# Optimization experiments

Measured on AMD Instinct MI355X. Metric: run time of the kernel, lower is better.

Reference implementation:

```python
import jax, jax.numpy as jnp
import numpy as np

E = 64          # num_experts
D_IN = 512      # in_features
D_OUT = 512     # out_features
T = 262144      # total routed token-slots (grouped by expert, balanced)


def setup_inputs() -> dict:
    key = jax.random.key(0)
    k1, k2 = jax.random.split(key)
    STD = 0.02
    return {
        "input": jax.random.normal(k1, (T, D_IN), dtype=jnp.float32),
        # tokens are pre-grouped by expert; balanced routing -> equal counts
        "num_experts_per_token": jnp.full((E,), T // E, dtype=jnp.int64),
        "weight": jax.random.normal(k2, (E, D_OUT, D_IN), dtype=jnp.float32) * STD,
        "bias": jnp.zeros((E, D_OUT), dtype=jnp.float32),
    }


def reference(input, num_experts_per_token, weight, bias):
    # Faithful to the split + per-expert F.linear + cat path, for balanced
    # routing (equal counts per expert) so shapes are static under jit.
    e = weight.shape[0]
    tpe = input.shape[0] // e  # tokens per expert
    x = input.reshape(e, tpe, -1)                      # [E, tpe, D_in]
    # F.linear(x_e, W_e) = x_e @ W_e.T for each expert -> grouped GEMM
    out = jnp.einsum('eti,eoi->eto', x, weight)        # [E, tpe, D_out]
    out = out + bias[:, None, :]
    return out.reshape(e * tpe, -1)                    # [T, D_out]
```

## Files before the change

kernel.cpp:

```cpp
#include <hip/hip_runtime.h>
#include <hip/hip_bf16.h>


#define NEXPERT 64
#define DIN 512
#define DOUT 512
#define TPE 4096
#define BM 128
#define BN 256
#define BK 32
#define NKT (DIN / BK)

typedef __attribute__((ext_vector_type(8))) __bf16 bf16x8;
typedef __attribute__((ext_vector_type(4))) __bf16 bf16x4;
typedef __attribute__((ext_vector_type(4))) float f32x4;

__global__ __launch_bounds__(256, 2)
void moe_grouped_gemm(const float* __restrict__ x,
                      const float* __restrict__ w,
                      const float* __restrict__ bias,
                      float* __restrict__ out) {
  __shared__ __align__(16) unsigned char sA[2][BM * BK * 2];
  __shared__ __align__(16) unsigned char sB[2][BN * BK * 2];

  int bid = blockIdx.x;
  int swz = (bid & 7) * 512 + (bid >> 3);
  int e  = swz >> 6;
  int rr = swz & 63;
  int mt = rr >> 1;
  int nt = rr & 1;

  const int tid  = threadIdx.x;
  const int lane = tid & 63;
  const int wn   = tid >> 6;
  const int r15  = lane & 15;
  const int kg   = lane >> 4;

  const int c4 = tid & 7;
  const int tr = tid >> 3;
  const float* aG = x + ((size_t)e * TPE + (size_t)mt * BM + tr) * DIN + c4 * 4;
  const float* bG = w + ((size_t)e * DOUT + (size_t)nt * BN + tr) * DIN + c4 * 4;
  const int wrBase = tr * 64 + ((((c4 >> 1) ^ ((tr >> 1) & 3))) << 4) + (c4 & 1) * 8;

  const int chz = (kg ^ ((r15 >> 1) & 3)) << 4;
  const int aRd = r15 * 64 + chz;
  const int bRd = (wn * 64 + r15) * 64 + chz;

  f32x4 SA[4], SBv[8];

#define ISSUE(kt)                                                           \
  do {                                                                      \
    _Pragma("unroll") for (int i = 0; i < 4; ++i)                           \
      SA[i] = *(const f32x4*)(aG + (size_t)i * 32 * DIN + (kt) * BK);       \
    _Pragma("unroll") for (int i = 0; i < 8; ++i)                           \
      SBv[i] = *(const f32x4*)(bG + (size_t)i * 32 * DIN + (kt) * BK);      \
  } while (0)

#define WRITE(dbuf)                                                         \
  do {                                                                      \
    _Pragma("unroll") for (int i = 0; i < 4; ++i) {                         \
      bf16x4 c;                                                             \
      c[0] = (__bf16)SA[i][0]; c[1] = (__bf16)SA[i][1];                     \
      c[2] = (__bf16)SA[i][2]; c[3] = (__bf16)SA[i][3];                     \
      *(bf16x4*)(&sA[dbuf][wrBase + i * 2048]) = c;                         \
    }                                                                       \
    _Pragma("unroll") for (int i = 0; i < 8; ++i) {                         \
      bf16x4 c;                                                             \
      c[0] = (__bf16)SBv[i][0]; c[1] = (__bf16)SBv[i][1];                   \
      c[2] = (__bf16)SBv[i][2]; c[3] = (__bf16)SBv[i][3];                   \
      *(bf16x4*)(&sB[dbuf][wrBase + i * 2048]) = c;                         \
    }                                                                       \
  } while (0)

  f32x4 acc[8][4];
#pragma unroll
  for (int m = 0; m < 8; ++m)
#pragma unroll
    for (int n = 0; n < 4; ++n) acc[m][n] = (f32x4)0.f;

  ISSUE(0);
  WRITE(0);
  asm volatile("s_waitcnt lgkmcnt(0)" ::: "memory");
  __builtin_amdgcn_s_barrier();

#pragma unroll
  for (int t = 0; t < NKT; ++t) {
    const int d = t & 1;
    bf16x8 bfr[4], afl[4], afh[4];

#pragma unroll
    for (int ni = 0; ni < 4; ++ni)
      bfr[ni] = *(const bf16x8*)(&sB[d][bRd + ni * 1024]);
#pragma unroll
    for (int mi = 0; mi < 4; ++mi)
      afl[mi] = *(const bf16x8*)(&sA[d][aRd + mi * 1024]);
    if (t + 1 < NKT) ISSUE(t + 1);

    __builtin_amdgcn_s_barrier();
    __builtin_amdgcn_s_setprio(1);
#pragma unroll
    for (int mi = 0; mi < 4; ++mi)
#pragma unroll
      for (int ni = 0; ni < 4; ++ni)
        acc[mi][ni] = __builtin_amdgcn_mfma_f32_16x16x32_bf16(
            afl[mi], bfr[ni], acc[mi][ni], 0, 0, 0);
    __builtin_amdgcn_s_setprio(0);
    __builtin_amdgcn_s_barrier();

#pragma unroll
    for (int mi = 0; mi < 4; ++mi)
      afh[mi] = *(const bf16x8*)(&sA[d][aRd + 4096 + mi * 1024]);
    if (t + 1 < NKT) WRITE(d ^ 1);

    asm volatile("s_waitcnt lgkmcnt(0)" ::: "memory");
    __builtin_amdgcn_s_barrier();
    __builtin_amdgcn_s_setprio(1);
#pragma unroll
    for (int mi = 0; mi < 4; ++mi)
#pragma unroll
      for (int ni = 0; ni < 4; ++ni)
        acc[mi + 4][ni] = __builtin_amdgcn_mfma_f32_16x16x32_bf16(
            afh[mi], bfr[ni], acc[mi + 4][ni], 0, 0, 0);
    __builtin_amdgcn_s_setprio(0);
    __builtin_amdgcn_s_barrier();
  }

  float bv[4];
  const float* bp = bias + (size_t)e * DOUT + nt * BN + wn * 64 + r15;
#pragma unroll
  for (int n = 0; n < 4; ++n) bv[n] = bp[n * 16];

  const int q4 = (lane >> 4) * 4;
  float* Cb = out + ((size_t)e * TPE + (size_t)mt * BM) * DOUT + nt * BN + wn * 64;
#pragma unroll
  for (int m = 0; m < 8; ++m) {
#pragma unroll
    for (int j = 0; j < 4; ++j) {
      float* pr = Cb + (size_t)(m * 16 + q4 + j) * DOUT;
#pragma unroll
      for (int n = 0; n < 4; ++n)
        pr[n * 16 + r15] = acc[m][n][j] + bv[n];
    }
  }
#undef ISSUE
#undef WRITE
}

extern "C" void kernel_launch(void* const* d_in, const int* in_sizes, int n_in,
                              void* d_out, int out_size, void* d_ws, size_t ws_size,
                              hipStream_t stream) {
  const float* x    = (const float*)d_in[0];
  const float* w    = (const float*)d_in[2];
  const float* bias = (const float*)d_in[3];
  float* out        = (float*)d_out;

  dim3 grid(NEXPERT * (TPE / BM) * (DOUT / BN));
  dim3 block(256);
  hipLaunchKernelGGL(moe_grouped_gemm, grid, block, 0, stream, x, w, bias, out);
}
```

Measured before the change: 305.3 us.

## Pre-convert weights to bf16 and load B fragments directly into registers

Adds a pre-pass kernel that converts the fp32 expert weights to bf16 in workspace. The GEMM then loads B fragments straight from global memory into registers instead of staging them through LDS, and shares a single LDS barrier per k-step with A prefetched two steps ahead. This is meant to cut LDS traffic, barriers and conversion work in the main loop. The cost is an extra launch and roughly 32MB of extra weight traffic, plus global B reads that are not shared across the waves of a block.

```diff
diff --git a/kernel.cpp b/kernel.cpp
--- a/kernel.cpp
+++ b/kernel.cpp
@@ -15,18 +15,27 @@
 typedef __attribute__((ext_vector_type(4))) __bf16 bf16x4;
 typedef __attribute__((ext_vector_type(4))) float f32x4;
 
+__global__ __launch_bounds__(256)
+void convert_w_kernel(const float* __restrict__ w, __bf16* __restrict__ wb) {
+  size_t i = ((size_t)blockIdx.x * 256 + threadIdx.x) * 8;
+  f32x4 a = *(const f32x4*)(w + i);
+  f32x4 b = *(const f32x4*)(w + i + 4);
+  bf16x8 r;
+  r[0] = (__bf16)a[0]; r[1] = (__bf16)a[1]; r[2] = (__bf16)a[2]; r[3] = (__bf16)a[3];
+  r[4] = (__bf16)b[0]; r[5] = (__bf16)b[1]; r[6] = (__bf16)b[2]; r[7] = (__bf16)b[3];
+  *(bf16x8*)(wb + i) = r;
+}
+
+template <bool WB16>
 __global__ __launch_bounds__(256, 2)
-void moe_grouped_gemm(const float* __restrict__ x,
-                      const float* __restrict__ w,
-                      const float* __restrict__ bias,
-                      float* __restrict__ out) {
+void moe_gemm(const float* __restrict__ x, const void* __restrict__ wsrc,
+              const float* __restrict__ bias, float* __restrict__ out) {
   __shared__ __align__(16) unsigned char sA[2][BM * BK * 2];
-  __shared__ __align__(16) unsigned char sB[2][BN * BK * 2];
 
   int bid = blockIdx.x;
-  int swz = (bid & 7) * 512 + (bid >> 3);
-  int e  = swz >> 6;
-  int rr = swz & 63;
+  int swzb = (bid & 7) * 512 + (bid >> 3);
+  int e  = swzb >> 6;
+  int rr = swzb & 63;
   int mt = rr >> 1;
   int nt = rr & 1;
 
@@ -39,38 +48,47 @@
   const int c4 = tid & 7;
   const int tr = tid >> 3;
   const float* aG = x + ((size_t)e * TPE + (size_t)mt * BM + tr) * DIN + c4 * 4;
-  const float* bG = w + ((size_t)e * DOUT + (size_t)nt * BN + tr) * DIN + c4 * 4;
-  const int wrBase = tr * 64 + ((((c4 >> 1) ^ ((tr >> 1) & 3))) << 4) + (c4 & 1) * 8;
+  const int wrBase = tr * 64 + (((c4 >> 1) ^ ((tr >> 1) & 3)) << 4) + (c4 & 1) * 8;
 
   const int chz = (kg ^ ((r15 >> 1) & 3)) << 4;
   const int aRd = r15 * 64 + chz;
-  const int bRd = (wn * 64 + r15) * 64 + chz;
 
-  f32x4 SA[4], SBv[8];
+  const size_t bRow = (size_t)(e * DOUT + nt * BN + wn * 64 + r15) * DIN + kg * 8;
+  const __bf16* bPb = (const __bf16*)wsrc + bRow;
+  const float*  bPf = (const float*)wsrc + bRow;
 
-#define ISSUE(kt)                                                           \
-  do {                                                                      \
-    _Pragma("unroll") for (int i = 0; i < 4; ++i)                           \
-      SA[i] = *(const f32x4*)(aG + (size_t)i * 32 * DIN + (kt) * BK);       \
-    _Pragma("unroll") for (int i = 0; i < 8; ++i)                           \
-      SBv[i] = *(const f32x4*)(bG + (size_t)i * 32 * DIN + (kt) * BK);      \
-  } while (0)
+  f32x4 sa0[4], sa1[4];
+  bf16x8 b0v[4], b1v[4];
 
-#define WRITE(dbuf)                                                         \
-  do {                                                                      \
-    _Pragma("unroll") for (int i = 0; i < 4; ++i) {                         \
+#define ISSUEA(kt, Sr)                                                      \
+  { _Pragma("unroll") for (int i = 0; i < 4; ++i)                           \
+      Sr[i] = *(const f32x4*)(aG + (size_t)i * 32 * DIN + (kt) * BK); }
+
+#define WRITEA(dbuf, Sr)                                                    \
+  { _Pragma("unroll") for (int i = 0; i < 4; ++i) {                         \
       bf16x4 c;                                                             \
-      c[0] = (__bf16)SA[i][0]; c[1] = (__bf16)SA[i][1];                     \
-      c[2] = (__bf16)SA[i][2]; c[3] = (__bf16)SA[i][3];                     \
-      *(bf16x4*)(&sA[dbuf][wrBase + i * 2048]) = c;                         \
-    }                                                                       \
-    _Pragma("unroll") for (int i = 0; i < 8; ++i) {                         \
-      bf16x4 c;                                                             \
-      c[0] = (__bf16)SBv[i][0]; c[1] = (__bf16)SBv[i][1];                   \
-      c[2] = (__bf16)SBv[i][2]; c[3] = (__bf16)SBv[i][3];                   \
-      *(bf16x4*)(&sB[dbuf][wrBase + i * 2048]) = c;                         \
-    }                                                                       \
-  } while (0)
+      c[0] = (__bf16)Sr[i][0]; c[1] = (__bf16)Sr[i][1];                     \
+      c[2] = (__bf16)Sr[i][2]; c[3] = (__bf16)Sr[i][3];                     \
+      *(bf16x4*)(&sA[dbuf][wrBase + i * 2048]) = c; } }
+
+#define LOADB(kt, Br)                                                       \
+  { if constexpr (WB16) {                                                   \
+      _Pragma("unroll") for (int n = 0; n < 4; ++n)                         \
+        Br[n] = *(const bf16x8*)(bPb + (size_t)n * 16 * DIN + (kt) * BK);   \
+    } else {                                                                \
+      _Pragma("unroll") for (int n = 0; n < 4; ++n) {                       \
+        f32x4 lo = *(const f32x4*)(bPf + (size_t)n * 16 * DIN + (kt) * BK); \
+        f32x4 hi = *(const f32x4*)(bPf + (size_t)n * 16 * DIN + (kt) * BK + 4); \
+        bf16x8 rv;                                                          \
+        rv[0]=(__bf16)lo[0]; rv[1]=(__bf16)lo[1]; rv[2]=(__bf16)lo[2]; rv[3]=(__bf16)lo[3]; \
+        rv[4]=(__bf16)hi[0]; rv[5]=(__bf16)hi[1]; rv[6]=(__bf16)hi[2]; rv[7]=(__bf16)hi[3]; \
+        Br[n] = rv; } } }
+
+#define MFMAS(Bv)                                                           \
+  { _Pragma("unroll") for (int mi = 0; mi < 8; ++mi)                        \
+      _Pragma("unroll") for (int ni = 0; ni < 4; ++ni)                      \
+        acc[mi][ni] = __builtin_amdgcn_mfma_f32_16x16x32_bf16(              \
+            af[mi], Bv[ni], acc[mi][ni], 0, 0, 0); }
 
   f32x4 acc[8][4];
 #pragma unroll
@@ -78,51 +96,41 @@
 #pragma unroll
     for (int n = 0; n < 4; ++n) acc[m][n] = (f32x4)0.f;
 
-  ISSUE(0);
-  WRITE(0);
+  ISSUEA(0, sa0);
+  ISSUEA(1, sa1);
+  LOADB(0, b0v);
+  WRITEA(0, sa0);
   asm volatile("s_waitcnt lgkmcnt(0)" ::: "memory");
   __builtin_amdgcn_s_barrier();
 
 #pragma unroll
   for (int t = 0; t < NKT; ++t) {
     const int d = t & 1;
-    bf16x8 bfr[4], afl[4], afh[4];
+    bf16x8 af[8];
+#pragma unroll
+    for (int mi = 0; mi < 8; ++mi)
+      af[mi] = *(const bf16x8*)(&sA[d][aRd + mi * 1024]);
 
-#pragma unroll
-    for (int ni = 0; ni < 4; ++ni)
-      bfr[ni] = *(const bf16x8*)(&sB[d][bRd + ni * 1024]);
-#pragma unroll
-    for (int mi = 0; mi < 4; ++mi)
-      afl[mi] = *(const bf16x8*)(&sA[d][aRd + mi * 1024]);
-    if (t + 1 < NKT) ISSUE(t + 1);
+    if (d == 0) {
+      if (t + 1 < NKT) LOADB(t + 1, b1v);
+      if (t + 2 < NKT) ISSUEA(t + 2, sa0);
+      if (t + 1 < NKT) WRITEA(1, sa1);
+      __builtin_amdgcn_s_setprio(1);
+      MFMAS(b0v);
+      __builtin_amdgcn_s_setprio(0);
+    } else {
+      if (t + 1 < NKT) LOADB(t + 1, b0v);
+      if (t + 2 < NKT) ISSUEA(t + 2, sa1);
+      if (t + 1 < NKT) WRITEA(0, sa0);
+      __builtin_amdgcn_s_setprio(1);
+      MFMAS(b1v);
+      __builtin_amdgcn_s_setprio(0);
+    }
 
-    __builtin_amdgcn_s_barrier();
-    __builtin_amdgcn_s_setprio(1);
-#pragma unroll
-    for (int mi = 0; mi < 4; ++mi)
-#pragma unroll
-      for (int ni = 0; ni < 4; ++ni)
-        acc[mi][ni] = __builtin_amdgcn_mfma_f32_16x16x32_bf16(
-            afl[mi], bfr[ni], acc[mi][ni], 0, 0, 0);
-    __builtin_amdgcn_s_setprio(0);
-    __builtin_amdgcn_s_barrier();
-
-#pragma unroll
-    for (int mi = 0; mi < 4; ++mi)
-      afh[mi] = *(const bf16x8*)(&sA[d][aRd + 4096 + mi * 1024]);
-    if (t + 1 < NKT) WRITE(d ^ 1);
-
-    asm volatile("s_waitcnt lgkmcnt(0)" ::: "memory");
-    __builtin_amdgcn_s_barrier();
-    __builtin_amdgcn_s_setprio(1);
-#pragma unroll
-    for (int mi = 0; mi < 4; ++mi)
-#pragma unroll
-      for (int ni = 0; ni < 4; ++ni)
-        acc[mi + 4][ni] = __builtin_amdgcn_mfma_f32_16x16x32_bf16(
-            afh[mi], bfr[ni], acc[mi + 4][ni], 0, 0, 0);
-    __builtin_amdgcn_s_setprio(0);
-    __builtin_amdgcn_s_barrier();
+    if (t + 1 < NKT) {
+      asm volatile("s_waitcnt lgkmcnt(0)" ::: "memory");
+      __builtin_amdgcn_s_barrier();
+    }
   }
 
   float bv[4];
@@ -142,8 +150,10 @@
         pr[n * 16 + r15] = acc[m][n][j] + bv[n];
     }
   }
-#undef ISSUE
-#undef WRITE
+#undef ISSUEA
+#undef WRITEA
+#undef LOADB
+#undef MFMAS
 }
 
 extern "C" void kernel_launch(void* const* d_in, const int* in_sizes, int n_in,
@@ -154,7 +164,19 @@
   const float* bias = (const float*)d_in[3];
   float* out        = (float*)d_out;
 
+  const size_t wElems = (size_t)NEXPERT * DOUT * DIN;
+  const size_t needWs = wElems * sizeof(__hip_bfloat16);
   dim3 grid(NEXPERT * (TPE / BM) * (DOUT / BN));
   dim3 block(256);
-  hipLaunchKernelGGL(moe_grouped_gemm, grid, block, 0, stream, x, w, bias, out);
+
+  if (ws_size >= needWs) {
+    dim3 cgrid(wElems / 8 / 256);
+    hipLaunchKernelGGL(convert_w_kernel, cgrid, block, 0, stream,
+                       w, (__bf16*)d_ws);
+    hipLaunchKernelGGL(moe_gemm<true>, grid, block, 0, stream,
+                       x, (const void*)d_ws, bias, out);
+  } else {
+    hipLaunchKernelGGL(moe_gemm<false>, grid, block, 0, stream,
+                       x, (const void*)w, bias, out);
+  }
 }
```

Result: slower. 339.6 us (+11.3%).
